# Optimization experiments

Hardware: AMD Instinct MI355X
Metric: run time of the kernel (lower is better)

## Reference

```python
import jax, jax.numpy as jnp
import numpy as np

D_MODEL = 1024
NUM_HEADS = 16


def setup_inputs() -> dict:
    key = jax.random.key(0)
    ks = jax.random.split(key, 11)
    B, S, D = 2, 2048, D_MODEL
    s = 1.0 / np.sqrt(D)
    return {
        "queries": jax.random.normal(ks[0], (B, S, D), jnp.float32),
        "keys": jax.random.normal(ks[1], (B, S, D), jnp.float32),
        "values": jax.random.normal(ks[2], (B, S, D), jnp.float32),
        "W_q": jax.random.normal(ks[3], (D, D), jnp.float32) * s,
        "b_q": jnp.zeros((D,), jnp.float32),
        "W_k": jax.random.normal(ks[4], (D, D), jnp.float32) * s,
        "b_k": jnp.zeros((D,), jnp.float32),
        "W_v": jax.random.normal(ks[5], (D, D), jnp.float32) * s,
        "b_v": jnp.zeros((D,), jnp.float32),
        "W_o": jax.random.normal(ks[6], (D, D), jnp.float32) * s,
        "b_o": jnp.zeros((D,), jnp.float32),
    }


def _split_heads(x, num_heads):
    # [B, S, D] -> [B, H, S, d_h]
    B, S, D = x.shape
    return x.reshape(B, S, num_heads, D // num_heads).transpose(0, 2, 1, 3)


def reference(queries, keys, values, W_q, b_q, W_k, b_k, W_v, b_v, W_o, b_o):
    H = NUM_HEADS
    Q = _split_heads(queries @ W_q.T + b_q, H)  # [B,H,S,dh]
    K = _split_heads(keys @ W_k.T + b_k, H)
    V = _split_heads(values @ W_v.T + b_v, H)
    d = Q.shape[-1]
    scores = jnp.einsum("bhqd,bhkd->bhqk", Q, K) / jnp.sqrt(jnp.asarray(d, Q.dtype))
    attn = jax.nn.softmax(scores, axis=-1)
    out = jnp.einsum("bhqk,bhkd->bhqd", attn, V)  # [B,H,S,dh]
    B, _, S, _ = out.shape
    out = out.transpose(0, 2, 1, 3).reshape(B, S, -1)  # combine heads
    return out @ W_o.T + b_o
```

## Files before the change

### kernel.cpp

```cpp
#include <hip/hip_runtime.h>
#include <cstdint>
#include <cmath>

typedef short s16x8 __attribute__((ext_vector_type(8)));
typedef short s16x4 __attribute__((ext_vector_type(4)));
typedef float f32x4 __attribute__((ext_vector_type(4)));
typedef unsigned int u32;

#define AS_G __attribute__((address_space(1)))
#define AS_L __attribute__((address_space(3)))

__device__ __forceinline__ void ld16_to_lds(const void* g, const void* l) {
    __builtin_amdgcn_global_load_lds((AS_G void*)(g), (AS_L void*)(l), 16, 0, 0);
}

__device__ __forceinline__ short f2bf(float f) {
    union { float f; uint32_t u; } v; v.f = f;
    uint32_t r = v.u + 0x7fffu + ((v.u >> 16) & 1u);
    return (short)(r >> 16);
}
__device__ __forceinline__ short f2bf_fast(float f) {
    union { float f; uint32_t u; } v; v.f = f;
    return (short)((v.u + 0x8000u) >> 16);
}

template<int F32OUT, int NJ>
__global__ __launch_bounds__(256, 3)
void gemm_bt(const short* __restrict__ Abase, long Az,
             const short* __restrict__ Wbase, long Wz,
             const float* __restrict__ bias0, const float* __restrict__ bias1,
             const float* __restrict__ bias2,
             void* __restrict__ Obase, long Oz,
             const int M, const int N, const int K)
{
    constexpr int BN = NJ * 32;
    constexpr int BSt = (BN * 4) / 256;
    __shared__ __align__(16) short As[4 * 128 * 8];
    __shared__ __align__(16) short Bs[4 * BN * 8];

    const int t = threadIdx.x, lane = t & 63, wv = t >> 6;
    const int wr = wv >> 1, wc = wv & 1;
    const int q4 = lane >> 4, l16 = lane & 15;
    const int z = blockIdx.z;
    const short* A  = Abase + (long)z * Az;
    const short* Bt = Wbase + (long)z * Wz;
    const float* bias = (z == 0) ? bias0 : ((z == 1) ? bias1 : bias2);
    const int bn0 = blockIdx.x * BN, bm0 = blockIdx.y * 128;

    f32x4 acc[4][NJ] = {};

    const short* gA[2];
    const short* gB[BSt];
    #pragma unroll
    for (int s = 0; s < 2; ++s) {
        const int c = t + 256 * s;
        gA[s] = A + (size_t)(bm0 + (c & 127)) * K + (c >> 7) * 8;
    }
    #pragma unroll
    for (int s = 0; s < BSt; ++s) {
        const int c = t + 256 * s;
        gB[s] = Bt + (size_t)(bn0 + (c & (BN - 1))) * K + (c / BN) * 8;
    }

    const int kIters = K >> 5;
    for (int kt = 0; kt < kIters; ++kt) {
        __syncthreads();
        #pragma unroll
        for (int s = 0; s < 2; ++s) {
            ld16_to_lds(gA[s], &As[(wv * 64 + 256 * s) * 8]);
            gA[s] += 32;
        }
        #pragma unroll
        for (int s = 0; s < BSt; ++s) {
            ld16_to_lds(gB[s], &Bs[(wv * 64 + 256 * s) * 8]);
            gB[s] += 32;
        }
        __syncthreads();

        s16x8 aF[4], bF[NJ];
        #pragma unroll
        for (int i = 0; i < 4; ++i)
            aF[i] = *(const s16x8*)&As[(q4 * 128 + wr * 64 + i * 16 + l16) * 8];
        #pragma unroll
        for (int j = 0; j < NJ; ++j)
            bF[j] = *(const s16x8*)&Bs[(q4 * BN + wc * (BN / 2) + j * 16 + l16) * 8];
        #pragma unroll
        for (int i = 0; i < 4; ++i)
            #pragma unroll
            for (int j = 0; j < NJ; ++j)
                acc[i][j] = __builtin_amdgcn_mfma_f32_16x16x32_bf16(
                    aF[i], bF[j], acc[i][j], 0, 0, 0);
    }

    #pragma unroll
    for (int j = 0; j < NJ; ++j) {
        const int col = bn0 + wc * (BN / 2) + j * 16 + l16;
        const float bj = bias[col];
        #pragma unroll
        for (int i = 0; i < 4; ++i) {
            const int row0 = bm0 + wr * 64 + i * 16 + q4 * 4;
            #pragma unroll
            for (int r = 0; r < 4; ++r) {
                const float v = acc[i][j][r] + bj;
                if (F32OUT)
                    ((float*)Obase + (long)z * Oz)[(size_t)(row0 + r) * N + col] = v;
                else
                    ((short*)Obase + (long)z * Oz)[(size_t)(row0 + r) * N + col] = f2bf(v);
            }
        }
    }
}

__global__ __launch_bounds__(256, 2)
void attn_fwd(const short* __restrict__ Qp, const short* __restrict__ Kp,
              const short* __restrict__ Vp, short* __restrict__ Out)
{
    constexpr int D = 1024, S = 2048;
    __shared__ __align__(16) short Ks[2][512 * 8];
    __shared__ __align__(16) short Vt[2][64 * 64];
    __shared__ __align__(16) short Ps[4 * 32 * 72];

    const int t = threadIdx.x, lane = t & 63, wv = t >> 6;
    const int q4 = lane >> 4, l16 = lane & 15;
    const int bid = blockIdx.x;
    const int qt = (bid >> 3) & 15;
    const int hb = (bid & 7) * 4 + (bid >> 7);
    const int h = hb >> 1, b = hb & 1;
    const size_t rowB = (size_t)b * S;
    const int cb = h * 64;
    const int qrow0 = qt * 128 + wv * 32;
    short* PsW = &Ps[wv * (32 * 72)];

    const int vl = t & 15, dc = (t >> 4) & 7, hf = t >> 7;

    s16x8 qF[2][2];
    #pragma unroll
    for (int i = 0; i < 2; ++i)
        #pragma unroll
        for (int tk = 0; tk < 2; ++tk)
            qF[i][tk] = *(const s16x8*)
                &Qp[(rowB + qrow0 + i * 16 + l16) * D + cb + tk * 32 + q4 * 8];

    f32x4 oacc[2][4] = {};
    float lrun[2][4] = {};
    const float sc = 0.125f * 1.44269504088896f;

    const short* KpB = Kp + rowB * D + cb;
    const short* VpB = Vp + rowB * D + cb + dc * 8;

    s16x8 va, vb;
    {
        #pragma unroll
        for (int s = 0; s < 2; ++s)
            ld16_to_lds(KpB + (size_t)lane * D + (wv + 4 * s) * 8,
                        &Ks[0][(wv * 64 + 256 * s) * 8]);
        const short* vsrc = VpB + (size_t)(vl + 32 * hf) * D;
        va = *(const s16x8*)vsrc;
        vb = *(const s16x8*)(vsrc + 16 * D);
        #pragma unroll
        for (int e = 0; e < 8; ++e) {
            const int d = dc * 8 + e;
            const int cp = (vl * 4 + 2 * hf) ^ ((d & 7) * 8);
            *(u32*)&Vt[0][d * 64 + cp] =
                ((u32)(unsigned short)va[e]) | ((u32)(unsigned short)vb[e] << 16);
        }
        const short* vsrc1 = VpB + (size_t)(64 + vl + 32 * hf) * D;
        va = *(const s16x8*)vsrc1;
        vb = *(const s16x8*)(vsrc1 + 16 * D);
    }

    for (int kvt = 0; kvt < 32; ++kvt) {
        const int kv0 = kvt * 64;
        __syncthreads();
        if (kvt < 31) {
            #pragma unroll
            for (int s = 0; s < 2; ++s)
                ld16_to_lds(KpB + (size_t)(kv0 + 64 + lane) * D + (wv + 4 * s) * 8,
                            &Ks[(kvt + 1) & 1][(wv * 64 + 256 * s) * 8]);
            #pragma unroll
            for (int e = 0; e < 8; ++e) {
                const int d = dc * 8 + e;
                const int cp = (vl * 4 + 2 * hf) ^ ((d & 7) * 8);
                *(u32*)&Vt[(kvt + 1) & 1][d * 64 + cp] =
                    ((u32)(unsigned short)va[e]) | ((u32)(unsigned short)vb[e] << 16);
            }
        }
        if (kvt < 30) {
            const short* vsrc = VpB + (size_t)(kv0 + 128 + vl + 32 * hf) * D;
            va = *(const s16x8*)vsrc;
            vb = *(const s16x8*)(vsrc + 16 * D);
        }

        f32x4 acc[2][4] = {};
        #pragma unroll
        for (int tk = 0; tk < 2; ++tk) {
            s16x8 kF[4];
            #pragma unroll
            for (int j = 0; j < 4; ++j)
                kF[j] = *(const s16x8*)
                    &Ks[kvt & 1][((tk * 4 + q4) * 64 + j * 16 + l16) * 8];
            #pragma unroll
            for (int j = 0; j < 4; ++j) {
                acc[0][j] = __builtin_amdgcn_mfma_f32_16x16x32_bf16(
                    qF[0][tk], kF[j], acc[0][j], 0, 0, 0);
                acc[1][j] = __builtin_amdgcn_mfma_f32_16x16x32_bf16(
                    qF[1][tk], kF[j], acc[1][j], 0, 0, 0);
            }
        }

        #pragma unroll
        for (int i = 0; i < 2; ++i) {
            #pragma unroll
            for (int r = 0; r < 4; ++r) {
                const int m = i * 16 + q4 * 4 + r;
                s16x4 pv;
                float rs = 0.f;
                #pragma unroll
                for (int j = 0; j < 4; ++j) {
                    const float p = __builtin_amdgcn_exp2f(acc[i][j][r] * sc);
                    rs += p;
                    pv[j] = f2bf_fast(p);
                }
                *(s16x4*)&PsW[m * 72 + l16 * 4] = pv;
                lrun[i][r] += rs;
            }
        }

        #pragma unroll
        for (int tk = 0; tk < 2; ++tk) {
            const s16x8 pF0 = *(const s16x8*)&PsW[l16 * 72 + tk * 32 + q4 * 8];
            const s16x8 pF1 = *(const s16x8*)&PsW[(16 + l16) * 72 + tk * 32 + q4 * 8];
            #pragma unroll
            for (int jd = 0; jd < 4; ++jd) {
                const int d = jd * 16 + l16;
                const s16x8 vF = *(const s16x8*)
                    &Vt[kvt & 1][d * 64 + ((tk * 32 + q4 * 8) ^ ((d & 7) * 8))];
                oacc[0][jd] = __builtin_amdgcn_mfma_f32_16x16x32_bf16(
                    pF0, vF, oacc[0][jd], 0, 0, 0);
                oacc[1][jd] = __builtin_amdgcn_mfma_f32_16x16x32_bf16(
                    pF1, vF, oacc[1][jd], 0, 0, 0);
            }
        }
    }

    #pragma unroll
    for (int i = 0; i < 2; ++i) {
        #pragma unroll
        for (int r = 0; r < 4; ++r) {
            float lr = lrun[i][r];
            lr += __shfl_xor(lr, 1);
            lr += __shfl_xor(lr, 2);
            lr += __shfl_xor(lr, 4);
            lr += __shfl_xor(lr, 8);
            const float inv = 1.0f / lr;
            const size_t row = rowB + qrow0 + i * 16 + q4 * 4 + r;
            #pragma unroll
            for (int jd = 0; jd < 4; ++jd)
                Out[row * D + cb + jd * 16 + l16] = f2bf(oacc[i][jd][r] * inv);
        }
    }
}

__global__ __launch_bounds__(256)
void cast_all(const float* __restrict__ q, const float* __restrict__ k,
              const float* __restrict__ v, const float* __restrict__ wq,
              const float* __restrict__ wk, const float* __restrict__ wv,
              const float* __restrict__ wo, short* __restrict__ out)
{
    const size_t i = ((size_t)blockIdx.x * 256 + threadIdx.x) * 8;
    const float* src; size_t off;
    if      (i < 4194304)  { src = q;  off = i; }
    else if (i < 8388608)  { src = k;  off = i - 4194304; }
    else if (i < 12582912) { src = v;  off = i - 8388608; }
    else if (i < 13631488) { src = wq; off = i - 12582912; }
    else if (i < 14680064) { src = wk; off = i - 13631488; }
    else if (i < 15728640) { src = wv; off = i - 14680064; }
    else                   { src = wo; off = i - 15728640; }
    const float4 a = *(const float4*)(src + off);
    const float4 c = *(const float4*)(src + off + 4);
    s16x8 o;
    o[0] = f2bf(a.x); o[1] = f2bf(a.y); o[2] = f2bf(a.z); o[3] = f2bf(a.w);
    o[4] = f2bf(c.x); o[5] = f2bf(c.y); o[6] = f2bf(c.z); o[7] = f2bf(c.w);
    *(s16x8*)(out + i) = o;
}

extern "C" void kernel_launch(void* const* d_in, const int* in_sizes, int n_in,
                              void* d_out, int out_size, void* d_ws, size_t ws_size,
                              hipStream_t stream)
{
    const float* q  = (const float*)d_in[0];
    const float* k  = (const float*)d_in[1];
    const float* v  = (const float*)d_in[2];
    const float* Wq = (const float*)d_in[3];
    const float* bq = (const float*)d_in[4];
    const float* Wk = (const float*)d_in[5];
    const float* bk = (const float*)d_in[6];
    const float* Wv = (const float*)d_in[7];
    const float* bv = (const float*)d_in[8];
    const float* Wo = (const float*)d_in[9];
    const float* bo = (const float*)d_in[10];

    short* ws = (short*)d_ws;
    const long MEL = 1048576;
    short* Aq  = ws;
    short* Wqb = ws + 12 * MEL;
    short* Wob = ws + 15 * MEL;
    short* Qp  = ws + 16 * MEL;
    short* Kp  = ws + 20 * MEL;
    short* Vp  = ws + 24 * MEL;
    short* AO  = ws;

    cast_all<<<8192, 256, 0, stream>>>(q, k, v, Wq, Wk, Wv, Wo, ws);

    gemm_bt<0, 4><<<dim3(8, 32, 3), 256, 0, stream>>>(
        Aq, 4 * MEL, Wqb, 1 * MEL, bq, bk, bv, Qp, 4 * MEL, 4096, 1024, 1024);

    attn_fwd<<<512, 256, 0, stream>>>(Qp, Kp, Vp, AO);

    gemm_bt<1, 2><<<dim3(16, 32, 1), 256, 0, stream>>>(
        AO, 0, Wob, 0, bo, bo, bo, d_out, 0, 4096, 1024, 1024);
}
```

Measured before the change: 266.2 us.

## Store V transposed from projection, fold softmax scale into Wq, MFMA row sums

The QKV projection now writes V transposed (feature-major), so the attention kernel can stream V tiles straight into LDS with async global-to-LDS loads instead of register loads and scalar transposing stores. The softmax scale and log2e factor are folded into W_q and b_q during the cast, which removes a multiply per score. Row sums are accumulated with an extra MFMA against a ones vector instead of scalar adds plus cross-lane shuffles. The row sums now come from the bf16-rounded probabilities, and the transposed V store in the GEMM epilogue uses strided 8-byte writes that may coalesce poorly.

Measured after the change: 260.4 us. 2.2% less time.

```diff
diff --git a/kernel.cpp b/kernel.cpp
--- a/kernel.cpp
+++ b/kernel.cpp
@@ -10,6 +10,8 @@
 #define AS_G __attribute__((address_space(1)))
 #define AS_L __attribute__((address_space(3)))
 
+#define QSCALE 0.18033688011112042f
+
 __device__ __forceinline__ void ld16_to_lds(const void* g, const void* l) {
     __builtin_amdgcn_global_load_lds((AS_G void*)(g), (AS_L void*)(l), 16, 0, 0);
 }
@@ -24,7 +26,7 @@
     return (short)((v.u + 0x8000u) >> 16);
 }
 
-template<int F32OUT, int NJ>
+template<int F32OUT, int NJ, int QKV>
 __global__ __launch_bounds__(256, 3)
 void gemm_bt(const short* __restrict__ Abase, long Az,
              const short* __restrict__ Wbase, long Wz,
@@ -45,6 +47,7 @@
     const short* A  = Abase + (long)z * Az;
     const short* Bt = Wbase + (long)z * Wz;
     const float* bias = (z == 0) ? bias0 : ((z == 1) ? bias1 : bias2);
+    const float bmul = (QKV && z == 0) ? QSCALE : 1.0f;
     const int bn0 = blockIdx.x * BN, bm0 = blockIdx.y * 128;
 
     f32x4 acc[4][NJ] = {};
@@ -95,17 +98,25 @@
     #pragma unroll
     for (int j = 0; j < NJ; ++j) {
         const int col = bn0 + wc * (BN / 2) + j * 16 + l16;
-        const float bj = bias[col];
+        const float bj = bias[col] * bmul;
         #pragma unroll
         for (int i = 0; i < 4; ++i) {
             const int row0 = bm0 + wr * 64 + i * 16 + q4 * 4;
-            #pragma unroll
-            for (int r = 0; r < 4; ++r) {
-                const float v = acc[i][j][r] + bj;
-                if (F32OUT)
-                    ((float*)Obase + (long)z * Oz)[(size_t)(row0 + r) * N + col] = v;
-                else
-                    ((short*)Obase + (long)z * Oz)[(size_t)(row0 + r) * N + col] = f2bf(v);
+            if (QKV && z == 2) {
+                s16x4 ov;
+                #pragma unroll
+                for (int r = 0; r < 4; ++r) ov[r] = f2bf(acc[i][j][r] + bj);
+                *(s16x4*)(((short*)Obase + (long)z * Oz) +
+                          (size_t)col * 4096 + row0) = ov;
+            } else {
+                #pragma unroll
+                for (int r = 0; r < 4; ++r) {
+                    const float v = acc[i][j][r] + bj;
+                    if (F32OUT)
+                        ((float*)Obase + (long)z * Oz)[(size_t)(row0 + r) * N + col] = v;
+                    else
+                        ((short*)Obase + (long)z * Oz)[(size_t)(row0 + r) * N + col] = f2bf(v);
+                }
             }
         }
     }
@@ -113,11 +124,11 @@
 
 __global__ __launch_bounds__(256, 2)
 void attn_fwd(const short* __restrict__ Qp, const short* __restrict__ Kp,
-              const short* __restrict__ Vp, short* __restrict__ Out)
+              const short* __restrict__ VpT, short* __restrict__ Out)
 {
     constexpr int D = 1024, S = 2048;
     __shared__ __align__(16) short Ks[2][512 * 8];
-    __shared__ __align__(16) short Vt[2][64 * 64];
+    __shared__ __align__(16) short Vt[2][512 * 8];
     __shared__ __align__(16) short Ps[4 * 32 * 72];
 
     const int t = threadIdx.x, lane = t & 63, wv = t >> 6;
@@ -131,7 +142,7 @@
     const int qrow0 = qt * 128 + wv * 32;
     short* PsW = &Ps[wv * (32 * 72)];
 
-    const int vl = t & 15, dc = (t >> 4) & 7, hf = t >> 7;
+    const int ksrow = 4 * l16 + q4;
 
     s16x8 qF[2][2];
     #pragma unroll
@@ -142,31 +153,25 @@
                 &Qp[(rowB + qrow0 + i * 16 + l16) * D + cb + tk * 32 + q4 * 8];
 
     f32x4 oacc[2][4] = {};
-    float lrun[2][4] = {};
-    const float sc = 0.125f * 1.44269504088896f;
+    f32x4 lacc[2] = {};
+    s16x8 onesF;
+    #pragma unroll
+    for (int e = 0; e < 8; ++e) onesF[e] = (short)0x3F80;
 
     const short* KpB = Kp + rowB * D + cb;
-    const short* VpB = Vp + rowB * D + cb + dc * 8;
-
-    s16x8 va, vb;
-    {
-        #pragma unroll
-        for (int s = 0; s < 2; ++s)
-            ld16_to_lds(KpB + (size_t)lane * D + (wv + 4 * s) * 8,
-                        &Ks[0][(wv * 64 + 256 * s) * 8]);
-        const short* vsrc = VpB + (size_t)(vl + 32 * hf) * D;
-        va = *(const s16x8*)vsrc;
-        vb = *(const s16x8*)(vsrc + 16 * D);
-        #pragma unroll
-        for (int e = 0; e < 8; ++e) {
-            const int d = dc * 8 + e;
-            const int cp = (vl * 4 + 2 * hf) ^ ((d & 7) * 8);
-            *(u32*)&Vt[0][d * 64 + cp] =
-                ((u32)(unsigned short)va[e]) | ((u32)(unsigned short)vb[e] << 16);
-        }
-        const short* vsrc1 = VpB + (size_t)(64 + vl + 32 * hf) * D;
-        va = *(const s16x8*)vsrc1;
-        vb = *(const s16x8*)(vsrc1 + 16 * D);
+    const short* VtG = VpT + (size_t)cb * 4096 + b * 2048;
+
+    #pragma unroll
+    for (int s = 0; s < 2; ++s) {
+        ld16_to_lds(KpB + (size_t)ksrow * D + (wv + 4 * s) * 8,
+                    &Ks[0][(wv * 64 + 256 * s) * 8]);
+    }
+    #pragma unroll
+    for (int s = 0; s < 2; ++s) {
+        const int c = t + 256 * s;
+        const int d = c >> 3, kcp = c & 7;
+        ld16_to_lds(VtG + (size_t)d * 4096 + ((kcp ^ (d & 7)) * 8),
+                    &Vt[0][(wv * 64 + 256 * s) * 8]);
     }
 
     for (int kvt = 0; kvt < 32; ++kvt) {
@@ -174,21 +179,17 @@
         __syncthreads();
         if (kvt < 31) {
             #pragma unroll
-            for (int s = 0; s < 2; ++s)
-                ld16_to_lds(KpB + (size_t)(kv0 + 64 + lane) * D + (wv + 4 * s) * 8,
+            for (int s = 0; s < 2; ++s) {
+                ld16_to_lds(KpB + (size_t)(kv0 + 64 + ksrow) * D + (wv + 4 * s) * 8,
                             &Ks[(kvt + 1) & 1][(wv * 64 + 256 * s) * 8]);
-            #pragma unroll
-            for (int e = 0; e < 8; ++e) {
-                const int d = dc * 8 + e;
-                const int cp = (vl * 4 + 2 * hf) ^ ((d & 7) * 8);
-                *(u32*)&Vt[(kvt + 1) & 1][d * 64 + cp] =
-                    ((u32)(unsigned short)va[e]) | ((u32)(unsigned short)vb[e] << 16);
-            }
-        }
-        if (kvt < 30) {
-            const short* vsrc = VpB + (size_t)(kv0 + 128 + vl + 32 * hf) * D;
-            va = *(const s16x8*)vsrc;
-            vb = *(const s16x8*)(vsrc + 16 * D);
+            }
+            #pragma unroll
+            for (int s = 0; s < 2; ++s) {
+                const int c = t + 256 * s;
+                const int d = c >> 3, kcp = c & 7;
+                ld16_to_lds(VtG + (size_t)d * 4096 + kv0 + 64 + ((kcp ^ (d & 7)) * 8),
+                            &Vt[(kvt + 1) & 1][(wv * 64 + 256 * s) * 8]);
+            }
         }
 
         f32x4 acc[2][4] = {};
@@ -214,15 +215,10 @@
             for (int r = 0; r < 4; ++r) {
                 const int m = i * 16 + q4 * 4 + r;
                 s16x4 pv;
-                float rs = 0.f;
                 #pragma unroll
-                for (int j = 0; j < 4; ++j) {
-                    const float p = __builtin_amdgcn_exp2f(acc[i][j][r] * sc);
-                    rs += p;
-                    pv[j] = f2bf_fast(p);
-                }
+                for (int j = 0; j < 4; ++j)
+                    pv[j] = f2bf_fast(__builtin_amdgcn_exp2f(acc[i][j][r]));
                 *(s16x4*)&PsW[m * 72 + l16 * 4] = pv;
-                lrun[i][r] += rs;
             }
         }
 
@@ -230,11 +226,15 @@
         for (int tk = 0; tk < 2; ++tk) {
             const s16x8 pF0 = *(const s16x8*)&PsW[l16 * 72 + tk * 32 + q4 * 8];
             const s16x8 pF1 = *(const s16x8*)&PsW[(16 + l16) * 72 + tk * 32 + q4 * 8];
+            lacc[0] = __builtin_amdgcn_mfma_f32_16x16x32_bf16(
+                pF0, onesF, lacc[0], 0, 0, 0);
+            lacc[1] = __builtin_amdgcn_mfma_f32_16x16x32_bf16(
+                pF1, onesF, lacc[1], 0, 0, 0);
             #pragma unroll
             for (int jd = 0; jd < 4; ++jd) {
                 const int d = jd * 16 + l16;
                 const s16x8 vF = *(const s16x8*)
-                    &Vt[kvt & 1][d * 64 + ((tk * 32 + q4 * 8) ^ ((d & 7) * 8))];
+                    &Vt[kvt & 1][(d * 8 + ((tk * 4 + q4) ^ (d & 7))) * 8];
                 oacc[0][jd] = __builtin_amdgcn_mfma_f32_16x16x32_bf16(
                     pF0, vF, oacc[0][jd], 0, 0, 0);
                 oacc[1][jd] = __builtin_amdgcn_mfma_f32_16x16x32_bf16(
@@ -247,12 +247,7 @@
     for (int i = 0; i < 2; ++i) {
         #pragma unroll
         for (int r = 0; r < 4; ++r) {
-            float lr = lrun[i][r];
-            lr += __shfl_xor(lr, 1);
-            lr += __shfl_xor(lr, 2);
-            lr += __shfl_xor(lr, 4);
-            lr += __shfl_xor(lr, 8);
-            const float inv = 1.0f / lr;
+            const float inv = 1.0f / lacc[i][r];
             const size_t row = rowB + qrow0 + i * 16 + q4 * 4 + r;
             #pragma unroll
             for (int jd = 0; jd < 4; ++jd)
@@ -276,11 +271,12 @@
     else if (i < 14680064) { src = wk; off = i - 13631488; }
     else if (i < 15728640) { src = wv; off = i - 14680064; }
     else                   { src = wo; off = i - 15728640; }
+    const float m = (i >= 12582912 && i < 13631488) ? QSCALE : 1.0f;
     const float4 a = *(const float4*)(src + off);
     const float4 c = *(const float4*)(src + off + 4);
     s16x8 o;
-    o[0] = f2bf(a.x); o[1] = f2bf(a.y); o[2] = f2bf(a.z); o[3] = f2bf(a.w);
-    o[4] = f2bf(c.x); o[5] = f2bf(c.y); o[6] = f2bf(c.z); o[7] = f2bf(c.w);
+    o[0] = f2bf(a.x * m); o[1] = f2bf(a.y * m); o[2] = f2bf(a.z * m); o[3] = f2bf(a.w * m);
+    o[4] = f2bf(c.x * m); o[5] = f2bf(c.y * m); o[6] = f2bf(c.z * m); o[7] = f2bf(c.w * m);
     *(s16x8*)(out + i) = o;
 }
 
@@ -307,16 +303,16 @@
     short* Wob = ws + 15 * MEL;
     short* Qp  = ws + 16 * MEL;
     short* Kp  = ws + 20 * MEL;
-    short* Vp  = ws + 24 * MEL;
+    short* VpT = ws + 24 * MEL;
     short* AO  = ws;
 
     cast_all<<<8192, 256, 0, stream>>>(q, k, v, Wq, Wk, Wv, Wo, ws);
 
-    gemm_bt<0, 4><<<dim3(8, 32, 3), 256, 0, stream>>>(
+    gemm_bt<0, 4, 1><<<dim3(8, 32, 3), 256, 0, stream>>>(
         Aq, 4 * MEL, Wqb, 1 * MEL, bq, bk, bv, Qp, 4 * MEL, 4096, 1024, 1024);
 
-    attn_fwd<<<512, 256, 0, stream>>>(Qp, Kp, Vp, AO);
-
-    gemm_bt<1, 2><<<dim3(16, 32, 1), 256, 0, stream>>>(
+    attn_fwd<<<512, 256, 0, stream>>>(Qp, Kp, VpT, AO);
+
+    gemm_bt<1, 2, 0><<<dim3(16, 32, 1), 256, 0, stream>>>(
         AO, 0, Wob, 0, bo, bo, bo, d_out, 0, 4096, 1024, 1024);
 }
```
